# Kernel optimization log

Hardware: AMD Instinct MI355X
Metric: run time of the kernel (lower is better)

Reference implementation:

```python
import jax, jax.numpy as jnp
import numpy as np

B, S, H = 8, 1024, 16
DV = 1024      # video_input_dim
LAT = 1024     # latent_dim
DQ = LAT // H  # query_dim = 64
DH = 64        # head_dim


def setup_inputs() -> dict:
    key = jax.random.key(0)
    ks = jax.random.split(key, 12)
    sc = lambda fan_in: 1.0 / np.sqrt(fan_in)
    return {
        "input": jax.random.normal(ks[0], (B, S, DV), jnp.float32),
        "latent": jax.random.normal(ks[1], (B, S, LAT), jnp.float32),
        "attention_mask": jax.random.randint(ks[2], (B * H, S, S), 0, 2, jnp.int32),
        "Wq": jax.random.normal(ks[3], (LAT, H * DQ), jnp.float32) * sc(LAT),
        "bq": jnp.zeros((H * DQ,), jnp.float32),
        "Wk": jax.random.normal(ks[4], (DV, H * DQ), jnp.float32) * sc(DV),
        "bk": jnp.zeros((H * DQ,), jnp.float32),
        "Wv": jax.random.normal(ks[5], (DV, H * DH), jnp.float32) * sc(DV),
        "bv": jnp.zeros((H * DH,), jnp.float32),
        "Wo": jax.random.normal(ks[6], (H * DH, LAT), jnp.float32) * sc(H * DH),
        "bo": jnp.zeros((LAT,), jnp.float32),
    }


def reference(input, latent, attention_mask, Wq, bq, Wk, bk, Wv, bv, Wo, bo):
    b, s, _ = input.shape
    # projections -> [b, h, s, d]
    q = (latent @ Wq + bq).reshape(b, s, H, DQ).transpose(0, 2, 1, 3)
    k = (input @ Wk + bk).reshape(b, s, H, DQ).transpose(0, 2, 1, 3)
    v = (input @ Wv + bv).reshape(b, s, H, DH).transpose(0, 2, 1, 3)
    # [b, h, s, s] score matrix (materialized, as in the original bmm)
    scores = jnp.einsum("bhqd,bhkd->bhqk", q, k) / jnp.sqrt(jnp.float32(DQ))
    mask = attention_mask.reshape(b, H, s, s)
    scores = jnp.where(mask == 0, -jnp.inf, scores)
    weights = jax.nn.softmax(scores, axis=-1)
    out = jnp.einsum("bhqk,bhkd->bhqd", weights, v)  # [b, h, s, dh]
    out = out.transpose(0, 2, 1, 3).reshape(b, s, H * DH)
    return out @ Wo + bo
```

## Files before the change

kernel.cpp:

```cpp
#include <hip/hip_runtime.h>
#include <hip/hip_bf16.h>
#include <stdint.h>

typedef __bf16 bf16;
typedef __bf16 bf16x8 __attribute__((ext_vector_type(8)));
typedef float f32x4 __attribute__((ext_vector_type(4)));
typedef unsigned short u16;
typedef unsigned short u16x4 __attribute__((ext_vector_type(4)));


__device__ __forceinline__ void gld16(const bf16* g, bf16* l) {
    __builtin_amdgcn_global_load_lds(
        (const __attribute__((address_space(1))) void*)g,
        (__attribute__((address_space(3))) void*)l, 16, 0, 0);
}

__global__ __launch_bounds__(256) void prep(
        const float* __restrict__ input, const float* __restrict__ latent,
        bf16* __restrict__ Xb, bf16* __restrict__ Lb,
        const float* __restrict__ w0, const float* __restrict__ w1,
        const float* __restrict__ w2, const float* __restrict__ w3,
        bf16* __restrict__ t0, bf16* __restrict__ t1,
        bf16* __restrict__ t2, bf16* __restrict__ t3) {
    __shared__ float tile[32][33];
    const int bid = blockIdx.x;
    const int tid = threadIdx.x;
    if (bid < 4096) {
        const float* src = (bid >> 11) ? latent : input;
        bf16* dst = (bid >> 11) ? Lb : Xb;
        const int nchunk = (8 * 1024 * 1024) / 4;
        for (int c = (bid & 2047) * 256 + tid; c < nchunk; c += 2048 * 256) {
            float4 v = *(const float4*)&src[(size_t)c * 4];
            u16x4 o;
            o[0] = __builtin_bit_cast(u16, (bf16)v.x);
            o[1] = __builtin_bit_cast(u16, (bf16)v.y);
            o[2] = __builtin_bit_cast(u16, (bf16)v.z);
            o[3] = __builtin_bit_cast(u16, (bf16)v.w);
            *(u16x4*)&dst[(size_t)c * 4] = o;
        }
    } else {
        const int tb = bid - 4096;
        const float* src; bf16* dst;
        switch (tb >> 10) {
            case 0:  src = w0; dst = t0; break;
            case 1:  src = w1; dst = t1; break;
            case 2:  src = w2; dst = t2; break;
            default: src = w3; dst = t3; break;
        }
        const int r  = tb & 1023;
        const int bx = r & 31, by = r >> 5;
        const int tx = tid & 31, ty = tid >> 5;
        const int x = bx * 32 + tx;
        const int y = by * 32 + ty;
        #pragma unroll
        for (int j = 0; j < 32; j += 8)
            tile[ty + j][tx] = src[(size_t)(y + j) * 1024 + x];
        __syncthreads();
        const int x2 = by * 32 + tx;
        const int y2 = bx * 32 + ty;
        #pragma unroll
        for (int j = 0; j < 32; j += 8)
            dst[(size_t)(y2 + j) * 1024 + x2] = (bf16)tile[tx][ty + j];
    }
}

template<int MODE>
__device__ __forceinline__ void gemm_core(const bf16* __restrict__ X,
                                          const bf16* __restrict__ Wt,
                                          const float* __restrict__ bias,
                                          void* __restrict__ outv,
                                          int m0, int n0, bf16* Al, bf16* Bl) {
    const int tid  = threadIdx.x;
    const int lane = tid & 63;
    const int w    = tid >> 6;
    const int wm   = (w & 1) * 64;
    const int wn   = (w >> 1) * 64;
    const int l15  = lane & 15;
    const int quad = lane >> 4;
    const int sw   = (l15 >> 1) & 3;

    f32x4 acc[4][4] = {};

    for (int kt = 0; kt < 1024; kt += 32) {
        __syncthreads();
        #pragma unroll
        for (int t = 0; t < 2; t++) {
            int c = (w * 2 + t) * 64 + lane;
            int row = c >> 2;
            int e   = (c & 3) ^ ((c >> 3) & 3);
            gld16(&X [(size_t)(m0 + row) * 1024 + kt + e * 8], &Al[(w * 2 + t) * 512]);
            gld16(&Wt[(size_t)(n0 + row) * 1024 + kt + e * 8], &Bl[(w * 2 + t) * 512]);
        }
        __syncthreads();
        bf16x8 a[4], b[4];
        #pragma unroll
        for (int i = 0; i < 4; i++)
            a[i] = *(const bf16x8*)&Al[(wm + i * 16 + l15) * 32 + (quad ^ sw) * 8];
        #pragma unroll
        for (int j = 0; j < 4; j++)
            b[j] = *(const bf16x8*)&Bl[(wn + j * 16 + l15) * 32 + (quad ^ sw) * 8];
        #pragma unroll
        for (int i = 0; i < 4; i++)
            #pragma unroll
            for (int j = 0; j < 4; j++)
                acc[i][j] = __builtin_amdgcn_mfma_f32_16x16x32_bf16(a[i], b[j], acc[i][j], 0, 0, 0);
    }

    float bv[4];
    #pragma unroll
    for (int j = 0; j < 4; j++) bv[j] = bias[n0 + wn + j * 16 + l15];

    #pragma unroll
    for (int i = 0; i < 4; i++) {
        int mbase = m0 + wm + i * 16 + quad * 4;
        #pragma unroll
        for (int j = 0; j < 4; j++) {
            int n = n0 + wn + j * 16 + l15;
            if (MODE == 2) {
                bf16* out = (bf16*)outv;
                int b = mbase >> 10, s = mbase & 1023;
                int h = n >> 6, d = n & 63;
                u16x4 pack;
                #pragma unroll
                for (int r = 0; r < 4; r++) {
                    bf16 v = (bf16)(acc[i][j][r] + bv[j]);
                    pack[r] = __builtin_bit_cast(u16, v);
                }
                *(u16x4*)&out[(((size_t)(b * 16 + h)) * 64 + d) * 1024 + s] = pack;
            } else if (MODE == 1) {
                bf16* out = (bf16*)outv;
                #pragma unroll
                for (int r = 0; r < 4; r++) {
                    int m = mbase + r;
                    int b = m >> 10, s = m & 1023;
                    int h = n >> 6, d = n & 63;
                    out[(((size_t)(b * 16 + h)) * 1024 + s) * 64 + d] =
                        (bf16)(acc[i][j][r] + bv[j]);
                }
            } else {
                float* out = (float*)outv;
                #pragma unroll
                for (int r = 0; r < 4; r++)
                    out[(size_t)(mbase + r) * 1024 + n] = acc[i][j][r] + bv[j];
            }
        }
    }
}

__global__ __launch_bounds__(256) void gemm_qkv(
        const bf16* __restrict__ Lb, const bf16* __restrict__ Xb,
        const bf16* __restrict__ Wqt, const bf16* __restrict__ Wkt,
        const bf16* __restrict__ Wvt,
        const float* __restrict__ bq, const float* __restrict__ bk,
        const float* __restrict__ bv,
        bf16* __restrict__ Qh, bf16* __restrict__ Kh, bf16* __restrict__ Vt) {
    __shared__ bf16 Al[128 * 32];
    __shared__ bf16 Bl[128 * 32];
    const int m0 = blockIdx.x * 128, n0 = blockIdx.y * 128;
    if (blockIdx.z == 0)      gemm_core<1>(Lb, Wqt, bq, Qh, m0, n0, Al, Bl);
    else if (blockIdx.z == 1) gemm_core<1>(Xb, Wkt, bk, Kh, m0, n0, Al, Bl);
    else                      gemm_core<2>(Xb, Wvt, bv, Vt, m0, n0, Al, Bl);
}

__global__ __launch_bounds__(256) void gemm_o(
        const bf16* __restrict__ Ob, const bf16* __restrict__ Wot,
        const float* __restrict__ bo, float* __restrict__ out) {
    __shared__ bf16 Al[128 * 32];
    __shared__ bf16 Bl[128 * 32];
    gemm_core<0>(Ob, Wot, bo, out, blockIdx.x * 128, blockIdx.y * 128, Al, Bl);
}

__global__ __launch_bounds__(256, 2) void attn(const bf16* __restrict__ Q,
                                               const bf16* __restrict__ K,
                                               const bf16* __restrict__ Vt,
                                               const int*  __restrict__ mask,
                                               bf16* __restrict__ O) {
    __shared__ bf16 Kl[3][4096];
    __shared__ bf16 Vl[3][4096];
    __shared__ bf16 Pl[4][32 * 68];

    const int tid  = threadIdx.x;
    const int lane = tid & 63;
    const int w    = tid >> 6;
    const int l15  = lane & 15;
    const int quad = lane >> 4;

    const int blk = blockIdx.x;
    const int bh  = (blk & 7) * 16 + (blk >> 6);
    const int q0  = ((blk >> 3) & 7) * 128;
    const int qrow0 = q0 + w * 32;

    const bf16* Kbh = K  + (size_t)bh * 65536;
    const bf16* Vbh = Vt + (size_t)bh * 65536;
    const int* mbase = mask + ((size_t)bh * 1024 + qrow0 + quad * 4) * 1024;

    const int c0 = (w * 2 + 0) * 64 + lane;
    const int c1 = (w * 2 + 1) * 64 + lane;
    const int swz = l15 & 7;

    #define STAGE_KV(kk, buf)                                                          \
        {                                                                              \
            int r0 = c0 >> 3, e0 = (c0 & 7) ^ (r0 & 7);                                \
            int r1 = c1 >> 3, e1 = (c1 & 7) ^ (r1 & 7);                                \
            gld16(&Kbh[(size_t)((kk) + r0) * 64 + e0 * 8], &Kl[buf][(w * 2 + 0) * 512]); \
            gld16(&Kbh[(size_t)((kk) + r1) * 64 + e1 * 8], &Kl[buf][(w * 2 + 1) * 512]); \
            gld16(&Vbh[(size_t)r0 * 1024 + (kk) + e0 * 8], &Vl[buf][(w * 2 + 0) * 512]); \
            gld16(&Vbh[(size_t)r1 * 1024 + (kk) + e1 * 8], &Vl[buf][(w * 2 + 1) * 512]); \
        }

    bf16x8 qa[2][2];
    #pragma unroll
    for (int rb = 0; rb < 2; rb++) {
        const bf16* Qb = Q + ((size_t)bh * 1024 + qrow0 + rb * 16 + l15) * 64;
        qa[rb][0] = *(const bf16x8*)&Qb[quad * 8];
        qa[rb][1] = *(const bf16x8*)&Qb[32 + quad * 8];
    }
    STAGE_KV(0, 0);
    int mn[2][4][4];
    #pragma unroll
    for (int rb = 0; rb < 2; rb++)
        #pragma unroll
        for (int r = 0; r < 4; r++)
            #pragma unroll
            for (int t = 0; t < 4; t++)
                mn[rb][r][t] = mbase[(size_t)(rb * 16 + r) * 1024 + t * 16 + l15];
    STAGE_KV(64, 1);

    f32x4 o[2][4] = {};
    float lsum[2][4] = {};
    bf16* Pw = Pl[w];
    int cur = 0, stg = 2;

    for (int it = 0; it < 16; it++) {
        asm volatile("s_waitcnt vmcnt(8)" ::: "memory");
        __builtin_amdgcn_s_barrier();
        __builtin_amdgcn_sched_barrier(0);

        int nib[2][4];
        #pragma unroll
        for (int rb = 0; rb < 2; rb++)
            #pragma unroll
            for (int r = 0; r < 4; r++)
                nib[rb][r] = (mn[rb][r][0] != 0) | ((mn[rb][r][1] != 0) << 1) |
                             ((mn[rb][r][2] != 0) << 2) | ((mn[rb][r][3] != 0) << 3);

        {
            const int kn1 = ((it + 1) & 15) * 64;
            #pragma unroll
            for (int rb = 0; rb < 2; rb++)
                #pragma unroll
                for (int r = 0; r < 4; r++)
                    #pragma unroll
                    for (int t = 0; t < 4; t++)
                        mn[rb][r][t] = mbase[(size_t)(rb * 16 + r) * 1024 + kn1 + t * 16 + l15];
        }
        STAGE_KV(((it + 2) & 15) * 64, stg);

        const bf16* Kc = Kl[cur];
        const bf16* Vc = Vl[cur];

        f32x4 s[2][4];
        __builtin_amdgcn_s_setprio(1);
        #pragma unroll
        for (int t = 0; t < 4; t++) {
            bf16x8 kb0 = *(const bf16x8*)&Kc[(t * 16 + l15) * 64 + ((0 + quad) ^ swz) * 8];
            bf16x8 kb1 = *(const bf16x8*)&Kc[(t * 16 + l15) * 64 + ((4 + quad) ^ swz) * 8];
            #pragma unroll
            for (int rb = 0; rb < 2; rb++) {
                f32x4 z = {};
                z = __builtin_amdgcn_mfma_f32_16x16x32_bf16(qa[rb][0], kb0, z, 0, 0, 0);
                z = __builtin_amdgcn_mfma_f32_16x16x32_bf16(qa[rb][1], kb1, z, 0, 0, 0);
                s[rb][t] = z;
            }
        }
        __builtin_amdgcn_s_setprio(0);

        #pragma unroll
        for (int rb = 0; rb < 2; rb++)
            #pragma unroll
            for (int t = 0; t < 4; t++)
                #pragma unroll
                for (int r = 0; r < 4; r++) {
                    float p = __expf(fmaf(s[rb][t][r], 0.125f, -12.0f));
                    p = ((nib[rb][r] >> t) & 1) ? p : 0.0f;
                    lsum[rb][r] += p;
                    Pw[(rb * 16 + quad * 4 + r) * 68 + t * 16 + l15] = (bf16)p;
                }

        bf16x8 pa[2][2];
        #pragma unroll
        for (int rb = 0; rb < 2; rb++) {
            pa[rb][0] = *(const bf16x8*)&Pw[(rb * 16 + l15) * 68 + quad * 8];
            pa[rb][1] = *(const bf16x8*)&Pw[(rb * 16 + l15) * 68 + 32 + quad * 8];
        }
        __builtin_amdgcn_s_setprio(1);
        #pragma unroll
        for (int nt = 0; nt < 4; nt++) {
            bf16x8 vb0 = *(const bf16x8*)&Vc[(nt * 16 + l15) * 64 + ((0 + quad) ^ swz) * 8];
            bf16x8 vb1 = *(const bf16x8*)&Vc[(nt * 16 + l15) * 64 + ((4 + quad) ^ swz) * 8];
            #pragma unroll
            for (int rb = 0; rb < 2; rb++) {
                o[rb][nt] = __builtin_amdgcn_mfma_f32_16x16x32_bf16(pa[rb][0], vb0, o[rb][nt], 0, 0, 0);
                o[rb][nt] = __builtin_amdgcn_mfma_f32_16x16x32_bf16(pa[rb][1], vb1, o[rb][nt], 0, 0, 0);
            }
        }
        __builtin_amdgcn_s_setprio(0);

        cur = (cur == 2) ? 0 : cur + 1;
        stg = (stg == 2) ? 0 : stg + 1;
    }
    #undef STAGE_KV

    const int b = bh >> 4, h = bh & 15;
    #pragma unroll
    for (int rb = 0; rb < 2; rb++)
        #pragma unroll
        for (int r = 0; r < 4; r++) {
            float l = lsum[rb][r];
            #pragma unroll
            for (int off = 1; off < 16; off <<= 1)
                l += __shfl_xor(l, off, 64);
            float inv = 1.0f / l;
            int srow = qrow0 + rb * 16 + quad * 4 + r;
            bf16* orow = O + ((size_t)(b * 1024 + srow)) * 1024 + h * 64;
            #pragma unroll
            for (int nt = 0; nt < 4; nt++)
                orow[nt * 16 + l15] = (bf16)(o[rb][nt][r] * inv);
        }
}

extern "C" void kernel_launch(void* const* d_in, const int* in_sizes, int n_in,
                              void* d_out, int out_size, void* d_ws, size_t ws_size,
                              hipStream_t stream) {
    const float* input  = (const float*)d_in[0];
    const float* latent = (const float*)d_in[1];
    const int*   mask   = (const int*)d_in[2];
    const float* Wq = (const float*)d_in[3];
    const float* bq = (const float*)d_in[4];
    const float* Wk = (const float*)d_in[5];
    const float* bk = (const float*)d_in[6];
    const float* Wv = (const float*)d_in[7];
    const float* bv = (const float*)d_in[8];
    const float* Wo = (const float*)d_in[9];
    const float* bo = (const float*)d_in[10];
    float* out = (float*)d_out;

    char* ws = (char*)d_ws;
    bf16* Xb  = (bf16*)(ws);
    bf16* Lb  = (bf16*)(ws + (16u << 20));
    bf16* Qh  = (bf16*)(ws + (32u << 20));
    bf16* Kh  = (bf16*)(ws + (48u << 20));
    bf16* Vt  = (bf16*)(ws + (64u << 20));
    bf16* Ob  = (bf16*)(ws + (80u << 20));
    bf16* Wqt = (bf16*)(ws + (96u << 20));
    bf16* Wkt = (bf16*)(ws + (98u << 20));
    bf16* Wvt = (bf16*)(ws + (100u << 20));
    bf16* Wot = (bf16*)(ws + (102u << 20));

    prep<<<dim3(8192, 1, 1), 256, 0, stream>>>(
        input, latent, Xb, Lb, Wq, Wk, Wv, Wo, Wqt, Wkt, Wvt, Wot);

    gemm_qkv<<<dim3(64, 8, 3), 256, 0, stream>>>(
        Lb, Xb, Wqt, Wkt, Wvt, bq, bk, bv, Qh, Kh, Vt);

    attn<<<dim3(1024, 1, 1), 256, 0, stream>>>(Qh, Kh, Vt, mask, Ob);

    gemm_o<<<dim3(64, 8, 1), 256, 0, stream>>>(Ob, Wot, bo, out);
}
```

Measured before the change: 895.3 us.

## Transpose score MFMA so mask loads vectorize to int4 and P stores pack

The QK^T MFMA operands are swapped so each lane holds four consecutive key columns of a single query row. That lets the attention mask be read with 16-byte int4 loads instead of scalar 4-byte gathers, and lets P be written to LDS as packed 4x bf16 stores. The per-row sum reduction shrinks to two cross-quad shuffles plus one broadcast shuffle per row. exp is rewritten as exp2 with prescaled constants. The main target is the mask traffic, which dominates bytes moved; the risk is extra shuffles and a changed LDS write pattern with possible bank conflicts.

```diff
diff --git a/kernel.cpp b/kernel.cpp
--- a/kernel.cpp
+++ b/kernel.cpp
@@ -192,7 +192,7 @@
 
     const bf16* Kbh = K  + (size_t)bh * 65536;
     const bf16* Vbh = Vt + (size_t)bh * 65536;
-    const int* mbase = mask + ((size_t)bh * 1024 + qrow0 + quad * 4) * 1024;
+    const int* mbase = mask + ((size_t)bh * 1024 + qrow0 + l15) * 1024 + quad * 4;
 
     const int c0 = (w * 2 + 0) * 64 + lane;
     const int c1 = (w * 2 + 1) * 64 + lane;
@@ -216,18 +216,16 @@
         qa[rb][1] = *(const bf16x8*)&Qb[32 + quad * 8];
     }
     STAGE_KV(0, 0);
-    int mn[2][4][4];
+    int4 mn4[2][4];
     #pragma unroll
     for (int rb = 0; rb < 2; rb++)
         #pragma unroll
-        for (int r = 0; r < 4; r++)
-            #pragma unroll
-            for (int t = 0; t < 4; t++)
-                mn[rb][r][t] = mbase[(size_t)(rb * 16 + r) * 1024 + t * 16 + l15];
+        for (int t = 0; t < 4; t++)
+            mn4[rb][t] = *(const int4*)&mbase[rb * 16 * 1024 + t * 16];
     STAGE_KV(64, 1);
 
     f32x4 o[2][4] = {};
-    float lsum[2][4] = {};
+    float lsum[2] = {};
     bf16* Pw = Pl[w];
     int cur = 0, stg = 2;
 
@@ -240,19 +238,17 @@
         #pragma unroll
         for (int rb = 0; rb < 2; rb++)
             #pragma unroll
-            for (int r = 0; r < 4; r++)
-                nib[rb][r] = (mn[rb][r][0] != 0) | ((mn[rb][r][1] != 0) << 1) |
-                             ((mn[rb][r][2] != 0) << 2) | ((mn[rb][r][3] != 0) << 3);
+            for (int t = 0; t < 4; t++)
+                nib[rb][t] = (mn4[rb][t].x != 0) | ((mn4[rb][t].y != 0) << 1) |
+                             ((mn4[rb][t].z != 0) << 2) | ((mn4[rb][t].w != 0) << 3);
 
         {
             const int kn1 = ((it + 1) & 15) * 64;
             #pragma unroll
             for (int rb = 0; rb < 2; rb++)
                 #pragma unroll
-                for (int r = 0; r < 4; r++)
-                    #pragma unroll
-                    for (int t = 0; t < 4; t++)
-                        mn[rb][r][t] = mbase[(size_t)(rb * 16 + r) * 1024 + kn1 + t * 16 + l15];
+                for (int t = 0; t < 4; t++)
+                    mn4[rb][t] = *(const int4*)&mbase[rb * 16 * 1024 + kn1 + t * 16];
         }
         STAGE_KV(((it + 2) & 15) * 64, stg);
 
@@ -268,8 +264,8 @@
             #pragma unroll
             for (int rb = 0; rb < 2; rb++) {
                 f32x4 z = {};
-                z = __builtin_amdgcn_mfma_f32_16x16x32_bf16(qa[rb][0], kb0, z, 0, 0, 0);
-                z = __builtin_amdgcn_mfma_f32_16x16x32_bf16(qa[rb][1], kb1, z, 0, 0, 0);
+                z = __builtin_amdgcn_mfma_f32_16x16x32_bf16(kb0, qa[rb][0], z, 0, 0, 0);
+                z = __builtin_amdgcn_mfma_f32_16x16x32_bf16(kb1, qa[rb][1], z, 0, 0, 0);
                 s[rb][t] = z;
             }
         }
@@ -278,14 +274,18 @@
         #pragma unroll
         for (int rb = 0; rb < 2; rb++)
             #pragma unroll
-            for (int t = 0; t < 4; t++)
+            for (int t = 0; t < 4; t++) {
+                u16x4 pk;
                 #pragma unroll
                 for (int r = 0; r < 4; r++) {
-                    float p = __expf(fmaf(s[rb][t][r], 0.125f, -12.0f));
-                    p = ((nib[rb][r] >> t) & 1) ? p : 0.0f;
-                    lsum[rb][r] += p;
-                    Pw[(rb * 16 + quad * 4 + r) * 68 + t * 16 + l15] = (bf16)p;
+                    float p = exp2f(fmaf(s[rb][t][r], 0.1803368801111204f,
+                                         -17.312340490667565f));
+                    p = ((nib[rb][t] >> r) & 1) ? p : 0.0f;
+                    lsum[rb] += p;
+                    pk[r] = __builtin_bit_cast(u16, (bf16)p);
                 }
+                *(u16x4*)&Pw[(rb * 16 + l15) * 68 + t * 16 + quad * 4] = pk;
+            }
 
         bf16x8 pa[2][2];
         #pragma unroll
@@ -313,20 +313,21 @@
 
     const int b = bh >> 4, h = bh & 15;
     #pragma unroll
-    for (int rb = 0; rb < 2; rb++)
+    for (int rb = 0; rb < 2; rb++) {
+        float l = lsum[rb];
+        l += __shfl_xor(l, 16, 64);
+        l += __shfl_xor(l, 32, 64);
+        float inv = 1.0f / l;
         #pragma unroll
         for (int r = 0; r < 4; r++) {
-            float l = lsum[rb][r];
-            #pragma unroll
-            for (int off = 1; off < 16; off <<= 1)
-                l += __shfl_xor(l, off, 64);
-            float inv = 1.0f / l;
+            float invr = __shfl(inv, (lane & 48) | (quad * 4 + r), 64);
             int srow = qrow0 + rb * 16 + quad * 4 + r;
             bf16* orow = O + ((size_t)(b * 1024 + srow)) * 1024 + h * 64;
             #pragma unroll
             for (int nt = 0; nt < 4; nt++)
-                orow[nt * 16 + l15] = (bf16)(o[rb][nt][r] * inv);
-        }
+                orow[nt * 16 + l15] = (bf16)(o[rb][nt][r] * invr);
+        }
+    }
 }
 
 extern "C" void kernel_launch(void* const* d_in, const int* in_sizes, int n_in,
```

Result: no change. 901.8 us (+0.7%).
